# Performance work log

Measured on AMD Instinct MI355X. Metric: run time of the kernel, lower is better.

The kernel has to match this reference:

```python
import jax, jax.numpy as jnp
import numpy as np

N, M = 50000, 32
HID, FILT, NBR = 128, 128, 64


def setup_inputs() -> dict:
    key = jax.random.key(0)
    ks = jax.random.split(key, 12)
    s = lambda fan_in: 1.0 / np.sqrt(fan_in)
    return {
        "node_repr": jax.random.normal(ks[0], (N, HID), dtype=jnp.float32),
        "nbr_fea": jax.random.normal(ks[1], (N, M, NBR), dtype=jnp.float32),
        "nbr_fea_idx": jax.random.randint(ks[2], (N, M), 0, N, dtype=jnp.int64),
        # filter_net: Linear(NBR, FILT) -> SiLU -> Linear(FILT, HID)
        "fw1": jax.random.uniform(ks[3], (NBR, FILT), jnp.float32, -s(NBR), s(NBR)),
        "fb1": jax.random.uniform(ks[4], (FILT,), jnp.float32, -s(NBR), s(NBR)),
        "fw2": jax.random.uniform(ks[5], (FILT, HID), jnp.float32, -s(FILT), s(FILT)),
        "fb2": jax.random.uniform(ks[6], (HID,), jnp.float32, -s(FILT), s(FILT)),
        # update: Linear(HID, HID) -> SiLU -> Linear(HID, HID)
        "uw1": jax.random.uniform(ks[7], (HID, HID), jnp.float32, -s(HID), s(HID)),
        "ub1": jax.random.uniform(ks[8], (HID,), jnp.float32, -s(HID), s(HID)),
        "uw2": jax.random.uniform(ks[9], (HID, HID), jnp.float32, -s(HID), s(HID)),
        "ub2": jax.random.uniform(ks[10], (HID,), jnp.float32, -s(HID), s(HID)),
    }


def reference(node_repr, nbr_fea, nbr_fea_idx, fw1, fb1, fw2, fb2, uw1, ub1, uw2, ub2):
    # gather neighbor representations: [N, M, HID]
    neighbor_repr = node_repr[nbr_fea_idx]
    # continuous filters from neighbor features: [N, M, HID]
    h = jax.nn.silu(jnp.einsum("nmf,fk->nmk", nbr_fea, fw1) + fb1)
    filters = jnp.einsum("nmk,kh->nmh", h, fw2) + fb2
    # filter-weighted sum over neighbors: [N, HID]
    message = jnp.sum(neighbor_repr * filters, axis=1)
    # update MLP
    u = jax.nn.silu(message @ uw1 + ub1)
    return u @ uw2 + ub2
```

## Files before the change

kernel.cpp:

```cpp
#include <hip/hip_runtime.h>


#define NN 50000
#define MM 32
#define HID 128
#define NBR 64

typedef __attribute__((ext_vector_type(4))) float f32x4;
typedef __attribute__((ext_vector_type(8))) short s16x8;
typedef __attribute__((ext_vector_type(4))) short s16x4;

__device__ __forceinline__ short f2bf(float x) {
  unsigned u = __builtin_bit_cast(unsigned, x);
  unsigned r = (u + 0x7FFFu + ((u >> 16) & 1u)) >> 16;
  return (short)r;
}

__device__ __forceinline__ float silu(float x) {
  return x / (1.0f + __expf(-x));
}

__device__ __forceinline__ float rowsum16(float x) {
  int v = __builtin_bit_cast(int, x);
  v = __builtin_bit_cast(int,
      __builtin_bit_cast(float, v) +
      __builtin_bit_cast(float, __builtin_amdgcn_update_dpp(0, v, 0xB1, 0xF, 0xF, false)));
  v = __builtin_bit_cast(int,
      __builtin_bit_cast(float, v) +
      __builtin_bit_cast(float, __builtin_amdgcn_update_dpp(0, v, 0x4E, 0xF, 0xF, false)));
  v = __builtin_bit_cast(int,
      __builtin_bit_cast(float, v) +
      __builtin_bit_cast(float, __builtin_amdgcn_update_dpp(0, v, 0x124, 0xF, 0xF, false)));
  v = __builtin_bit_cast(int,
      __builtin_bit_cast(float, v) +
      __builtin_bit_cast(float, __builtin_amdgcn_update_dpp(0, v, 0x128, 0xF, 0xF, false)));
  return __builtin_bit_cast(float, v);
}

__global__ __launch_bounds__(512, 2) void k_filter_message(
    const float* __restrict__ node_repr, const float* __restrict__ nbr_fea,
    const int* __restrict__ nbr_idx, const float* __restrict__ fw1,
    const float* __restrict__ fb1, const float* __restrict__ fw2,
    const float* __restrict__ fb2, float* __restrict__ msg_out)
{
  __shared__ __align__(16) short s_w1[128 * 72];
  __shared__ __align__(16) short s_w2[128 * 136];
  __shared__ float s_b1[128];
  __shared__ __align__(16) float s_b2[128];

  const int tid = threadIdx.x;
  for (int i = tid; i < 64 * 128; i += 512) {
    int k = i >> 7, f = i & 127;
    s_w1[f * 72 + k] = f2bf(fw1[i]);
  }
  for (int i = tid; i < 128 * 128; i += 512) {
    int k = i >> 7, h = i & 127;
    s_w2[h * 136 + k] = f2bf(fw2[i]);
  }
  if (tid < 128) { s_b1[tid] = fb1[tid]; s_b2[tid] = fb2[tid]; }
  __syncthreads();

  const int wave = tid >> 6, lane = tid & 63;
  const int c = lane & 15, g = lane >> 4;
  const int gw = blockIdx.x * 8 + wave;
  const int stride = gridDim.x * 8;

  for (int n = gw; n < NN; n += stride) {
    const float* nf = nbr_fea + (size_t)n * (MM * NBR);

    int idx0 = nbr_idx[(size_t)n * MM + c];
    int idx1 = nbr_idx[(size_t)n * MM + 16 + c];

    s16x8 b1[2][2];
    #pragma unroll
    for (int mt = 0; mt < 2; ++mt)
      #pragma unroll
      for (int kt = 0; kt < 2; ++kt) {
        const f32x4* src = reinterpret_cast<const f32x4*>(
            nf + (mt * 16 + c) * NBR + kt * 32 + g * 8);
        f32x4 lo = __builtin_nontemporal_load(src);
        f32x4 hi = __builtin_nontemporal_load(src + 1);
        s16x8 v;
        v[0] = f2bf(lo[0]); v[1] = f2bf(lo[1]); v[2] = f2bf(lo[2]); v[3] = f2bf(lo[3]);
        v[4] = f2bf(hi[0]); v[5] = f2bf(hi[1]); v[6] = f2bf(hi[2]); v[7] = f2bf(hi[3]);
        b1[mt][kt] = v;
      }

    s16x4 P[8][2];
    #pragma unroll
    for (int t = 0; t < 8; ++t) {
      f32x4 a0 = f32x4{0.f, 0.f, 0.f, 0.f};
      f32x4 a1 = f32x4{0.f, 0.f, 0.f, 0.f};
      #pragma unroll
      for (int kt = 0; kt < 2; ++kt) {
        s16x8 w1f = *reinterpret_cast<const s16x8*>(&s_w1[(t * 16 + c) * 72 + kt * 32 + g * 8]);
        a0 = __builtin_amdgcn_mfma_f32_16x16x32_bf16(w1f, b1[0][kt], a0, 0, 0, 0);
        a1 = __builtin_amdgcn_mfma_f32_16x16x32_bf16(w1f, b1[1][kt], a1, 0, 0, 0);
      }
      s16x4 p0, p1;
      #pragma unroll
      for (int r = 0; r < 4; ++r) {
        float bias = s_b1[t * 16 + g * 4 + r];
        p0[r] = f2bf(silu(a0[r] + bias));
        p1[r] = f2bf(silu(a1[r] + bias));
      }
      P[t][0] = p0;
      P[t][1] = p1;
    }

    f32x4 pacc[8];
    #pragma unroll
    for (int ct = 0; ct < 8; ++ct) pacc[ct] = f32x4{0.f, 0.f, 0.f, 0.f};

    #pragma unroll
    for (int mt = 0; mt < 2; ++mt) {
      const float* nrp = node_repr + (size_t)(mt ? idx1 : idx0) * HID;
      #pragma unroll
      for (int ct = 0; ct < 8; ++ct) {
        f32x4 acc2t = f32x4{0.f, 0.f, 0.f, 0.f};
        #pragma unroll
        for (int kt = 0; kt < 8; ++kt) {
          s16x4 w2f = *reinterpret_cast<const s16x4*>(&s_w2[(ct * 16 + c) * 136 + kt * 16 + g * 4]);
          acc2t = __builtin_amdgcn_mfma_f32_16x16x16bf16_1k(w2f, P[kt][mt], acc2t, 0, 0, 0);
        }
        f32x4 nr = *reinterpret_cast<const f32x4*>(nrp + ct * 16 + 4 * g);
        f32x4 fb = *reinterpret_cast<const f32x4*>(&s_b2[ct * 16 + 4 * g]);
        #pragma unroll
        for (int r = 0; r < 4; ++r)
          pacc[ct][r] += (acc2t[r] + fb[r]) * nr[r];
      }
    }

    #pragma unroll
    for (int ct = 0; ct < 8; ++ct) {
      f32x4 s;
      #pragma unroll
      for (int r = 0; r < 4; ++r) s[r] = rowsum16(pacc[ct][r]);
      if (c == 0)
        *reinterpret_cast<f32x4*>(msg_out + (size_t)n * HID + ct * 16 + 4 * g) = s;
    }
  }
}

__global__ __launch_bounds__(256, 2) void k_update1(
    const float* __restrict__ msg, const float* __restrict__ uw1,
    const float* __restrict__ ub1, short* __restrict__ u_out)
{
  __shared__ __align__(16) short s_w1[128 * 136];
  __shared__ float s_b1[128];
  const int tid = threadIdx.x;
  for (int i = tid; i < 128 * 128; i += 256) {
    int k = i >> 7, f = i & 127;
    s_w1[f * 136 + k] = f2bf(uw1[i]);
  }
  if (tid < 128) s_b1[tid] = ub1[tid];
  __syncthreads();

  const int wave = tid >> 6, lane = tid & 63;
  const int c = lane & 15, g = lane >> 4;
  const long base = (long)(blockIdx.x * 4 + wave) * 32;
  if (base >= NN) return;

  s16x8 bfr[2][4];
  #pragma unroll
  for (int mt = 0; mt < 2; ++mt)
    #pragma unroll
    for (int kt = 0; kt < 4; ++kt) {
      long row = base + mt * 16 + c; if (row > NN - 1) row = NN - 1;
      const float* src = msg + row * HID + kt * 32 + g * 8;
      float4 lo = *reinterpret_cast<const float4*>(src);
      float4 hi = *reinterpret_cast<const float4*>(src + 4);
      s16x8 v;
      v[0] = f2bf(lo.x); v[1] = f2bf(lo.y); v[2] = f2bf(lo.z); v[3] = f2bf(lo.w);
      v[4] = f2bf(hi.x); v[5] = f2bf(hi.y); v[6] = f2bf(hi.z); v[7] = f2bf(hi.w);
      bfr[mt][kt] = v;
    }

  f32x4 acc[8][2];
  #pragma unroll
  for (int t = 0; t < 8; ++t)
    #pragma unroll
    for (int mt = 0; mt < 2; ++mt)
      acc[t][mt] = f32x4{0.f, 0.f, 0.f, 0.f};
  #pragma unroll
  for (int kt = 0; kt < 4; ++kt)
    #pragma unroll
    for (int t = 0; t < 8; ++t) {
      s16x8 a = *reinterpret_cast<const s16x8*>(&s_w1[(t * 16 + c) * 136 + kt * 32 + g * 8]);
      #pragma unroll
      for (int mt = 0; mt < 2; ++mt)
        acc[t][mt] = __builtin_amdgcn_mfma_f32_16x16x32_bf16(a, bfr[mt][kt], acc[t][mt], 0, 0, 0);
    }

  #pragma unroll
  for (int t = 0; t < 8; ++t)
    #pragma unroll
    for (int mt = 0; mt < 2; ++mt) {
      long row = base + mt * 16 + c;
      if (row < NN) {
        s16x4 p;
        #pragma unroll
        for (int r = 0; r < 4; ++r) {
          float x = acc[t][mt][r] + s_b1[t * 16 + g * 4 + r];
          p[r] = f2bf(silu(x));
        }
        *reinterpret_cast<s16x4*>(&u_out[row * HID + t * 16 + g * 4]) = p;
      }
    }
}

__global__ __launch_bounds__(256, 2) void k_update2(
    const short* __restrict__ u, const float* __restrict__ uw2,
    const float* __restrict__ ub2, float* __restrict__ out)
{
  __shared__ __align__(16) short s_w2[128 * 136];
  __shared__ float s_b2[128];
  const int tid = threadIdx.x;
  for (int i = tid; i < 128 * 128; i += 256) {
    int k = i >> 7, h = i & 127;
    s_w2[h * 136 + k] = f2bf(uw2[i]);
  }
  if (tid < 128) s_b2[tid] = ub2[tid];
  __syncthreads();

  const int wave = tid >> 6, lane = tid & 63;
  const int c = lane & 15, g = lane >> 4;
  const long base = (long)(blockIdx.x * 4 + wave) * 32;
  if (base >= NN) return;

  s16x4 afr[2][8];
  #pragma unroll
  for (int mt = 0; mt < 2; ++mt)
    #pragma unroll
    for (int kt = 0; kt < 8; ++kt) {
      long row = base + mt * 16 + c; if (row > NN - 1) row = NN - 1;
      afr[mt][kt] = *reinterpret_cast<const s16x4*>(&u[row * HID + kt * 16 + g * 4]);
    }

  f32x4 acc[8][2];
  #pragma unroll
  for (int ct = 0; ct < 8; ++ct)
    #pragma unroll
    for (int mt = 0; mt < 2; ++mt)
      acc[ct][mt] = f32x4{0.f, 0.f, 0.f, 0.f};
  #pragma unroll
  for (int ct = 0; ct < 8; ++ct)
    #pragma unroll
    for (int kt = 0; kt < 8; ++kt) {
      s16x4 b2 = *reinterpret_cast<const s16x4*>(&s_w2[(ct * 16 + c) * 136 + kt * 16 + g * 4]);
      #pragma unroll
      for (int mt = 0; mt < 2; ++mt)
        acc[ct][mt] = __builtin_amdgcn_mfma_f32_16x16x16bf16_1k(afr[mt][kt], b2, acc[ct][mt], 0, 0, 0);
    }

  #pragma unroll
  for (int ct = 0; ct < 8; ++ct) {
    const float bias = s_b2[ct * 16 + c];
    #pragma unroll
    for (int mt = 0; mt < 2; ++mt)
      #pragma unroll
      for (int r = 0; r < 4; ++r) {
        long row = base + mt * 16 + g * 4 + r;
        if (row < NN) out[row * HID + ct * 16 + c] = acc[ct][mt][r] + bias;
      }
  }
}

extern "C" void kernel_launch(void* const* d_in, const int* in_sizes, int n_in,
                              void* d_out, int out_size, void* d_ws, size_t ws_size,
                              hipStream_t stream) {
  const float* node_repr = (const float*)d_in[0];
  const float* nbr_fea   = (const float*)d_in[1];
  const int*   nbr_idx   = (const int*)d_in[2];
  const float* fw1 = (const float*)d_in[3];
  const float* fb1 = (const float*)d_in[4];
  const float* fw2 = (const float*)d_in[5];
  const float* fb2 = (const float*)d_in[6];
  const float* uw1 = (const float*)d_in[7];
  const float* ub1 = (const float*)d_in[8];
  const float* uw2 = (const float*)d_in[9];
  const float* ub2 = (const float*)d_in[10];
  float* outp = (float*)d_out;
  short* u_ws = (short*)d_ws;

  k_filter_message<<<512, 512, 0, stream>>>(node_repr, nbr_fea, nbr_idx,
                                            fw1, fb1, fw2, fb2, outp);
  const int rowblocks = (NN + 31) / 32;
  const int grid2 = (rowblocks + 3) / 4;
  k_update1<<<grid2, 256, 0, stream>>>(outp, uw1, ub1, u_ws);
  k_update2<<<grid2, 256, 0, stream>>>(u_ws, uw2, ub2, outp);
}
```

Baseline: 525.7 us.

## Software-pipeline neighbor feature loads and hoist gathers in filter-message kernel

Result: slower. 551.4 us (+4.9%).

```diff
diff --git a/kernel.cpp b/kernel.cpp
--- a/kernel.cpp
+++ b/kernel.cpp
@@ -63,29 +63,65 @@
   const int wave = tid >> 6, lane = tid & 63;
   const int c = lane & 15, g = lane >> 4;
   const int gw = blockIdx.x * 8 + wave;
-  const int stride = gridDim.x * 8;
-
-  for (int n = gw; n < NN; n += stride) {
-    const float* nf = nbr_fea + (size_t)n * (MM * NBR);
-
-    int idx0 = nbr_idx[(size_t)n * MM + c];
-    int idx1 = nbr_idx[(size_t)n * MM + 16 + c];
-
-    s16x8 b1[2][2];
+  const int STRIDE = 256 * 8;
+
+  f32x4 raw[8];
+  int idx0, idx1;
+  {
+    const float* nf = nbr_fea + (size_t)gw * (MM * NBR);
     #pragma unroll
     for (int mt = 0; mt < 2; ++mt)
       #pragma unroll
       for (int kt = 0; kt < 2; ++kt) {
         const f32x4* src = reinterpret_cast<const f32x4*>(
             nf + (mt * 16 + c) * NBR + kt * 32 + g * 8);
-        f32x4 lo = __builtin_nontemporal_load(src);
-        f32x4 hi = __builtin_nontemporal_load(src + 1);
+        raw[mt * 4 + kt * 2 + 0] = __builtin_nontemporal_load(src);
+        raw[mt * 4 + kt * 2 + 1] = __builtin_nontemporal_load(src + 1);
+      }
+    idx0 = nbr_idx[(size_t)gw * MM + c];
+    idx1 = nbr_idx[(size_t)gw * MM + 16 + c];
+  }
+
+  for (int n = gw; n < NN; n += STRIDE) {
+    int n2 = n + STRIDE; if (n2 >= NN) n2 = n;
+
+    const float* nrp0 = node_repr + (size_t)idx0 * HID;
+    const float* nrp1 = node_repr + (size_t)idx1 * HID;
+    f32x4 nr0[8], nr1[8];
+    #pragma unroll
+    for (int ct = 0; ct < 8; ++ct) {
+      nr0[ct] = *reinterpret_cast<const f32x4*>(nrp0 + ct * 16 + 4 * g);
+      nr1[ct] = *reinterpret_cast<const f32x4*>(nrp1 + ct * 16 + 4 * g);
+    }
+
+    s16x8 b1[2][2];
+    #pragma unroll
+    for (int mt = 0; mt < 2; ++mt)
+      #pragma unroll
+      for (int kt = 0; kt < 2; ++kt) {
+        f32x4 lo = raw[mt * 4 + kt * 2 + 0];
+        f32x4 hi = raw[mt * 4 + kt * 2 + 1];
         s16x8 v;
         v[0] = f2bf(lo[0]); v[1] = f2bf(lo[1]); v[2] = f2bf(lo[2]); v[3] = f2bf(lo[3]);
         v[4] = f2bf(hi[0]); v[5] = f2bf(hi[1]); v[6] = f2bf(hi[2]); v[7] = f2bf(hi[3]);
         b1[mt][kt] = v;
       }
 
+    {
+      const float* nf2 = nbr_fea + (size_t)n2 * (MM * NBR);
+      #pragma unroll
+      for (int mt = 0; mt < 2; ++mt)
+        #pragma unroll
+        for (int kt = 0; kt < 2; ++kt) {
+          const f32x4* src = reinterpret_cast<const f32x4*>(
+              nf2 + (mt * 16 + c) * NBR + kt * 32 + g * 8);
+          raw[mt * 4 + kt * 2 + 0] = __builtin_nontemporal_load(src);
+          raw[mt * 4 + kt * 2 + 1] = __builtin_nontemporal_load(src + 1);
+        }
+    }
+    int idx0n = nbr_idx[(size_t)n2 * MM + c];
+    int idx1n = nbr_idx[(size_t)n2 * MM + 16 + c];
+
     s16x4 P[8][2];
     #pragma unroll
     for (int t = 0; t < 8; ++t) {
@@ -110,25 +146,21 @@
 
     f32x4 pacc[8];
     #pragma unroll
-    for (int ct = 0; ct < 8; ++ct) pacc[ct] = f32x4{0.f, 0.f, 0.f, 0.f};
-
-    #pragma unroll
-    for (int mt = 0; mt < 2; ++mt) {
-      const float* nrp = node_repr + (size_t)(mt ? idx1 : idx0) * HID;
-      #pragma unroll
-      for (int ct = 0; ct < 8; ++ct) {
-        f32x4 acc2t = f32x4{0.f, 0.f, 0.f, 0.f};
-        #pragma unroll
-        for (int kt = 0; kt < 8; ++kt) {
-          s16x4 w2f = *reinterpret_cast<const s16x4*>(&s_w2[(ct * 16 + c) * 136 + kt * 16 + g * 4]);
-          acc2t = __builtin_amdgcn_mfma_f32_16x16x16bf16_1k(w2f, P[kt][mt], acc2t, 0, 0, 0);
-        }
-        f32x4 nr = *reinterpret_cast<const f32x4*>(nrp + ct * 16 + 4 * g);
-        f32x4 fb = *reinterpret_cast<const f32x4*>(&s_b2[ct * 16 + 4 * g]);
-        #pragma unroll
-        for (int r = 0; r < 4; ++r)
-          pacc[ct][r] += (acc2t[r] + fb[r]) * nr[r];
-      }
+    for (int ct = 0; ct < 8; ++ct) {
+      f32x4 t0 = f32x4{0.f, 0.f, 0.f, 0.f};
+      f32x4 t1 = f32x4{0.f, 0.f, 0.f, 0.f};
+      #pragma unroll
+      for (int kt = 0; kt < 8; ++kt) {
+        s16x4 w2f = *reinterpret_cast<const s16x4*>(&s_w2[(ct * 16 + c) * 136 + kt * 16 + g * 4]);
+        t0 = __builtin_amdgcn_mfma_f32_16x16x16bf16_1k(w2f, P[kt][0], t0, 0, 0, 0);
+        t1 = __builtin_amdgcn_mfma_f32_16x16x16bf16_1k(w2f, P[kt][1], t1, 0, 0, 0);
+      }
+      f32x4 fb = *reinterpret_cast<const f32x4*>(&s_b2[ct * 16 + 4 * g]);
+      f32x4 a;
+      #pragma unroll
+      for (int r = 0; r < 4; ++r)
+        a[r] = (t0[r] + fb[r]) * nr0[ct][r] + (t1[r] + fb[r]) * nr1[ct][r];
+      pacc[ct] = a;
     }
 
     #pragma unroll
@@ -139,6 +171,9 @@
       if (c == 0)
         *reinterpret_cast<f32x4*>(msg_out + (size_t)n * HID + ct * 16 + 4 * g) = s;
     }
+
+    idx0 = idx0n;
+    idx1 = idx1n;
   }
 }
 
@@ -283,7 +318,7 @@
   float* outp = (float*)d_out;
   short* u_ws = (short*)d_ws;
 
-  k_filter_message<<<512, 512, 0, stream>>>(node_repr, nbr_fea, nbr_idx,
+  k_filter_message<<<256, 512, 0, stream>>>(node_repr, nbr_fea, nbr_idx,
                                             fw1, fb1, fw2, fb2, outp);
   const int rowblocks = (NN + 31) / 32;
   const int grid2 = (rowblocks + 3) / 4;
```

## Gather bf16 node features, prefetch indices, and reshape filter-message launch

Applied to the files above, without the earlier changes.

Result: slower. 701.8 us (+33.5%).

```diff
diff --git a/kernel.cpp b/kernel.cpp
--- a/kernel.cpp
+++ b/kernel.cpp
@@ -14,6 +14,10 @@
   unsigned u = __builtin_bit_cast(unsigned, x);
   unsigned r = (u + 0x7FFFu + ((u >> 16) & 1u)) >> 16;
   return (short)r;
+}
+
+__device__ __forceinline__ float bf2f(short b) {
+  return __builtin_bit_cast(float, (unsigned)(unsigned short)b << 16);
 }
 
 __device__ __forceinline__ float silu(float x) {
@@ -37,8 +41,21 @@
   return __builtin_bit_cast(float, v);
 }
 
-__global__ __launch_bounds__(512, 2) void k_filter_message(
-    const float* __restrict__ node_repr, const float* __restrict__ nbr_fea,
+__global__ __launch_bounds__(256) void k_cvt_node(
+    const float* __restrict__ in, short* __restrict__ out)
+{
+  int i = blockIdx.x * 256 + threadIdx.x;
+  if (i < NN * HID / 4) {
+    f32x4 v = *(reinterpret_cast<const f32x4*>(in) + i);
+    s16x4 o;
+    #pragma unroll
+    for (int r = 0; r < 4; ++r) o[r] = f2bf(v[r]);
+    reinterpret_cast<s16x4*>(out)[i] = o;
+  }
+}
+
+__global__ __launch_bounds__(256, 3) void k_filter_message(
+    const short* __restrict__ node_bf, const float* __restrict__ nbr_fea,
     const int* __restrict__ nbr_idx, const float* __restrict__ fw1,
     const float* __restrict__ fb1, const float* __restrict__ fw2,
     const float* __restrict__ fb2, float* __restrict__ msg_out)
@@ -49,11 +66,11 @@
   __shared__ __align__(16) float s_b2[128];
 
   const int tid = threadIdx.x;
-  for (int i = tid; i < 64 * 128; i += 512) {
+  for (int i = tid; i < 64 * 128; i += 256) {
     int k = i >> 7, f = i & 127;
     s_w1[f * 72 + k] = f2bf(fw1[i]);
   }
-  for (int i = tid; i < 128 * 128; i += 512) {
+  for (int i = tid; i < 128 * 128; i += 256) {
     int k = i >> 7, h = i & 127;
     s_w2[h * 136 + k] = f2bf(fw2[i]);
   }
@@ -62,15 +79,23 @@
 
   const int wave = tid >> 6, lane = tid & 63;
   const int c = lane & 15, g = lane >> 4;
-  const int gw = blockIdx.x * 8 + wave;
-  const int stride = gridDim.x * 8;
-
-  for (int n = gw; n < NN; n += stride) {
+  const int gw = blockIdx.x * 4 + wave;
+  const int STRIDE = 1024 * 4;
+
+  int idx0 = nbr_idx[(size_t)gw * MM + c];
+  int idx1 = nbr_idx[(size_t)gw * MM + 16 + c];
+
+  for (int n = gw; n < NN; n += STRIDE) {
+    const short* nb0 = node_bf + (size_t)idx0 * HID;
+    const short* nb1 = node_bf + (size_t)idx1 * HID;
+    s16x4 nr0[8], nr1[8];
+    #pragma unroll
+    for (int ct = 0; ct < 8; ++ct) {
+      nr0[ct] = *reinterpret_cast<const s16x4*>(nb0 + ct * 16 + 4 * g);
+      nr1[ct] = *reinterpret_cast<const s16x4*>(nb1 + ct * 16 + 4 * g);
+    }
+
     const float* nf = nbr_fea + (size_t)n * (MM * NBR);
-
-    int idx0 = nbr_idx[(size_t)n * MM + c];
-    int idx1 = nbr_idx[(size_t)n * MM + 16 + c];
-
     s16x8 b1[2][2];
     #pragma unroll
     for (int mt = 0; mt < 2; ++mt)
@@ -86,6 +111,13 @@
         b1[mt][kt] = v;
       }
 
+    {
+      int n2 = n + STRIDE;
+      int np = (n2 < NN) ? n2 : n;
+      idx0 = nbr_idx[(size_t)np * MM + c];
+      idx1 = nbr_idx[(size_t)np * MM + 16 + c];
+    }
+
     s16x4 P[8][2];
     #pragma unroll
     for (int t = 0; t < 8; ++t) {
@@ -110,25 +142,22 @@
 
     f32x4 pacc[8];
     #pragma unroll
-    for (int ct = 0; ct < 8; ++ct) pacc[ct] = f32x4{0.f, 0.f, 0.f, 0.f};
-
-    #pragma unroll
-    for (int mt = 0; mt < 2; ++mt) {
-      const float* nrp = node_repr + (size_t)(mt ? idx1 : idx0) * HID;
-      #pragma unroll
-      for (int ct = 0; ct < 8; ++ct) {
-        f32x4 acc2t = f32x4{0.f, 0.f, 0.f, 0.f};
-        #pragma unroll
-        for (int kt = 0; kt < 8; ++kt) {
-          s16x4 w2f = *reinterpret_cast<const s16x4*>(&s_w2[(ct * 16 + c) * 136 + kt * 16 + g * 4]);
-          acc2t = __builtin_amdgcn_mfma_f32_16x16x16bf16_1k(w2f, P[kt][mt], acc2t, 0, 0, 0);
-        }
-        f32x4 nr = *reinterpret_cast<const f32x4*>(nrp + ct * 16 + 4 * g);
-        f32x4 fb = *reinterpret_cast<const f32x4*>(&s_b2[ct * 16 + 4 * g]);
-        #pragma unroll
-        for (int r = 0; r < 4; ++r)
-          pacc[ct][r] += (acc2t[r] + fb[r]) * nr[r];
-      }
+    for (int ct = 0; ct < 8; ++ct) {
+      f32x4 t0 = f32x4{0.f, 0.f, 0.f, 0.f};
+      f32x4 t1 = f32x4{0.f, 0.f, 0.f, 0.f};
+      #pragma unroll
+      for (int kt = 0; kt < 8; ++kt) {
+        s16x4 w2f = *reinterpret_cast<const s16x4*>(&s_w2[(ct * 16 + c) * 136 + kt * 16 + g * 4]);
+        t0 = __builtin_amdgcn_mfma_f32_16x16x16bf16_1k(w2f, P[kt][0], t0, 0, 0, 0);
+        t1 = __builtin_amdgcn_mfma_f32_16x16x16bf16_1k(w2f, P[kt][1], t1, 0, 0, 0);
+      }
+      f32x4 fb = *reinterpret_cast<const f32x4*>(&s_b2[ct * 16 + 4 * g]);
+      f32x4 a;
+      #pragma unroll
+      for (int r = 0; r < 4; ++r)
+        a[r] = (t0[r] + fb[r]) * bf2f(nr0[ct][r]) +
+               (t1[r] + fb[r]) * bf2f(nr1[ct][r]);
+      pacc[ct] = a;
     }
 
     #pragma unroll
@@ -281,12 +310,13 @@
   const float* uw2 = (const float*)d_in[9];
   const float* ub2 = (const float*)d_in[10];
   float* outp = (float*)d_out;
-  short* u_ws = (short*)d_ws;
-
-  k_filter_message<<<512, 512, 0, stream>>>(node_repr, nbr_fea, nbr_idx,
-                                            fw1, fb1, fw2, fb2, outp);
+  short* ws16 = (short*)d_ws;
+
+  k_cvt_node<<<(NN * HID / 4 + 255) / 256, 256, 0, stream>>>(node_repr, ws16);
+  k_filter_message<<<1024, 256, 0, stream>>>(ws16, nbr_fea, nbr_idx,
+                                             fw1, fb1, fw2, fb2, outp);
   const int rowblocks = (NN + 31) / 32;
   const int grid2 = (rowblocks + 3) / 4;
-  k_update1<<<grid2, 256, 0, stream>>>(outp, uw1, ub1, u_ws);
-  k_update2<<<grid2, 256, 0, stream>>>(u_ws, uw2, ub2, outp);
-}
+  k_update1<<<grid2, 256, 0, stream>>>(outp, uw1, ub1, ws16);
+  k_update2<<<grid2, 256, 0, stream>>>(ws16, uw2, ub2, outp);
+}
```
